# Kernel optimization log

Hardware: AMD Instinct MI355X
Metric: run time of the kernel (lower is better)

## Reference

```python
import jax, jax.numpy as jnp
import numpy as np

B, C, H, W = 64, 1, 512, 512
THRESHOLD = 50.0
LEVELS = 3


def _haar_dwt2(x):
    """Single-level 2D Haar DWT on [B,H,W] (even H,W). Returns (cA,(cH,cV,cD)).
    Matches pywt 'haar' coefficient magnitudes (sign conventions are irrelevant
    to the loss, which is odd-symmetric through soft-threshold and uses |.|)."""
    a = x[:, 0::2, 0::2]
    b = x[:, 0::2, 1::2]
    c = x[:, 1::2, 0::2]
    d = x[:, 1::2, 1::2]
    half = jnp.float32(0.5)
    cA = (a + b + c + d) * half
    cH = (a + b - c - d) * half  # low along cols, high along rows
    cV = (a - b + c - d) * half  # high along cols, low along rows
    cD = (a - b - c + d) * half  # high/high
    return cA, (cH, cV, cD)


def _wavedec2(x, levels):
    """Multi-level DWT. Returns detail tuples ordered coarsest-first,
    matching pywt.wavedec2 list order coeffs[1:]."""
    details = []
    cA = x
    for _ in range(levels):
        cA, d = _haar_dwt2(cA)
        details.append(d)
    details.reverse()  # coarsest first
    return details


def _soft_threshold(x, thr):
    return jnp.sign(x) * jnp.maximum(jnp.abs(x) - thr, 0.0)


def setup_inputs() -> dict:
    key = jax.random.key(0)
    k1, k2 = jax.random.split(key)
    pred = jax.random.uniform(k1, (B, C, H, W), dtype=jnp.float32)
    target = jax.random.uniform(k2, (B, C, H, W), dtype=jnp.float32)
    return {"pred": pred, "target": target}


def reference(pred, target):
    p = pred[:, 0]   # [B,H,W]
    t = target[:, 0]
    det_p = _wavedec2(p, LEVELS)
    det_t = _wavedec2(t, LEVELS)
    total = jnp.float32(0.0)
    for level_idx in range(1, LEVELS + 1):
        # per-level adaptive threshold, normalized to [0,1] image range
        thr = jnp.float32((THRESHOLD / 2.0 ** (level_idx - 1)) / 255.0)
        level_weight = jnp.float32(1.0 / level_idx)
        dp = det_p[level_idx - 1]
        dt = det_t[level_idx - 1]
        level_loss = jnp.float32(0.0)
        for k in range(3):  # cH, cV, cD
            diff = _soft_threshold(dp[k], thr) - _soft_threshold(dt[k], thr)
            level_loss = level_loss + jnp.mean(jnp.abs(diff))
        total = total + level_weight * level_loss / 3.0
    # per-sample sum / valid_samples == batch mean (all samples valid here)
    return total
```

## Files before the change

kernel.cpp:

```cpp
#include <hip/hip_runtime.h>


#define IMG_W 512
#define N_BATCH 64

#define THR1 (50.0f / 255.0f)
#define THR2 (25.0f / 255.0f)
#define THR3 (12.5f / 255.0f)

#define NBLK 1024
#define N_WAVES (NBLK * 4)
#define N_TILES 8192

__device__ __forceinline__ float softthr(float x, float thr) {
    float m = fmaxf(fabsf(x) - thr, 0.0f);
    return copysignf(m, x);
}

__device__ __forceinline__ float detail_term(float p, float t, float thr) {
    return fabsf(softthr(p, thr) - softthr(t, thr));
}

__device__ __forceinline__ void haar_quad(float a, float b, float c, float d,
                                          float& cA, float& cH, float& cV, float& cD) {
    cA = 0.5f * (a + b + c + d);
    cH = 0.5f * (a + b - c - d);
    cV = 0.5f * (a - b + c - d);
    cD = 0.5f * (a - b - c + d);
}

__device__ __forceinline__ float4 ld4(const float* p) { return *(const float4*)p; }

__global__ __launch_bounds__(256, 4)
void wavelet_main(const float* __restrict__ pred,
                  const float* __restrict__ target,
                  float* __restrict__ ws) {
    constexpr float W1 = 1.0f / (1.0f * 3.0f * (float)(N_BATCH * 256 * 256));
    constexpr float W2 = 1.0f / (2.0f * 3.0f * (float)(N_BATCH * 128 * 128));
    constexpr float W3 = 1.0f / (3.0f * 3.0f * (float)(N_BATCH * 64 * 64));

    const int wid = blockIdx.x * 4 + (threadIdx.x >> 6);
    const int li  = threadIdx.x & 63;

    float acc = 0.0f;

    #pragma unroll
    for (int t = 0; t < 2; ++t) {
        const int T     = wid + t * N_WAVES;
        const int img   = T >> 7;
        const int rem   = T & 127;
        const int half  = rem & 1;
        const int strip = rem >> 1;

        const size_t off = (size_t)img * (512 * 512)
                         + (size_t)strip * 8 * IMG_W
                         + half * 256 + 4 * li;
        const float* pb = pred + off;
        const float* tb = target + off;

        float4 Pa[2], Pb[2], Ta[2], Tb[2];
        Pa[0] = ld4(pb);            Pb[0] = ld4(pb + IMG_W);
        Ta[0] = ld4(tb);            Tb[0] = ld4(tb + IMG_W);
        Pa[1] = ld4(pb + 1024);     Pb[1] = ld4(pb + 1536);
        Ta[1] = ld4(tb + 1024);     Tb[1] = ld4(tb + 1536);

        float s1 = 0.0f, s2 = 0.0f;
        float cA1p[4][2], cA1t[4][2];

        #pragma unroll
        for (int rp = 0; rp < 4; ++rp) {
            const int bsel = rp & 1;
            const float4 p0 = Pa[bsel], p1 = Pb[bsel];
            const float4 q0 = Ta[bsel], q1 = Tb[bsel];

            if (rp < 2) {
                const int o = (rp + 2) * 1024;
                Pa[bsel] = ld4(pb + o);         Pb[bsel] = ld4(pb + o + IMG_W);
                Ta[bsel] = ld4(tb + o);         Tb[bsel] = ld4(tb + o + IMG_W);
            }

            float cA, cH, cV, cD, cAt, cHt, cVt, cDt;
            haar_quad(p0.x, p0.y, p1.x, p1.y, cA, cH, cV, cD);
            haar_quad(q0.x, q0.y, q1.x, q1.y, cAt, cHt, cVt, cDt);
            s1 += detail_term(cH, cHt, THR1) + detail_term(cV, cVt, THR1) + detail_term(cD, cDt, THR1);
            cA1p[rp][0] = cA; cA1t[rp][0] = cAt;
            haar_quad(p0.z, p0.w, p1.z, p1.w, cA, cH, cV, cD);
            haar_quad(q0.z, q0.w, q1.z, q1.w, cAt, cHt, cVt, cDt);
            s1 += detail_term(cH, cHt, THR1) + detail_term(cV, cVt, THR1) + detail_term(cD, cDt, THR1);
            cA1p[rp][1] = cA; cA1t[rp][1] = cAt;
        }

        float cA2p[2], cA2t[2];
        {
            float cH, cV, cD, cHt, cVt, cDt;
            haar_quad(cA1p[0][0], cA1p[0][1], cA1p[1][0], cA1p[1][1], cA2p[0], cH, cV, cD);
            haar_quad(cA1t[0][0], cA1t[0][1], cA1t[1][0], cA1t[1][1], cA2t[0], cHt, cVt, cDt);
            s2 += detail_term(cH, cHt, THR2) + detail_term(cV, cVt, THR2) + detail_term(cD, cDt, THR2);
            haar_quad(cA1p[2][0], cA1p[2][1], cA1p[3][0], cA1p[3][1], cA2p[1], cH, cV, cD);
            haar_quad(cA1t[2][0], cA1t[2][1], cA1t[3][0], cA1t[3][1], cA2t[1], cHt, cVt, cDt);
            s2 += detail_term(cH, cHt, THR2) + detail_term(cV, cVt, THR2) + detail_term(cD, cDt, THR2);
        }

        float s3;
        {
            const float bP = __shfl_xor(cA2p[0], 1);
            const float dP = __shfl_xor(cA2p[1], 1);
            const float bT = __shfl_xor(cA2t[0], 1);
            const float dT = __shfl_xor(cA2t[1], 1);
            float cA, cH, cV, cD, cAt, cHt, cVt, cDt;
            haar_quad(cA2p[0], bP, cA2p[1], dP, cA, cH, cV, cD);
            haar_quad(cA2t[0], bT, cA2t[1], dT, cAt, cHt, cVt, cDt);
            s3 = detail_term(cH, cHt, THR3) + detail_term(cV, cVt, THR3) + detail_term(cD, cDt, THR3);
        }
        const float w3 = (li & 1) ? 0.0f : W3;

        acc += W1 * s1 + W2 * s2 + w3 * s3;
    }

    #pragma unroll
    for (int off = 32; off > 0; off >>= 1)
        acc += __shfl_down(acc, off, 64);

    __shared__ float wave_sums[4];
    const int lane_b = threadIdx.x & 63;
    const int wave_b = threadIdx.x >> 6;
    if (lane_b == 0) wave_sums[wave_b] = acc;
    __syncthreads();
    if (threadIdx.x == 0)
        ws[blockIdx.x] = wave_sums[0] + wave_sums[1] + wave_sums[2] + wave_sums[3];
}

__global__ __launch_bounds__(256)
void wavelet_reduce(const float* __restrict__ ws, float* __restrict__ out) {
    const int tidx = threadIdx.x;
    float v = 0.0f;
    #pragma unroll
    for (int k = 0; k < NBLK / 256; ++k)
        v += ws[tidx + k * 256];

    #pragma unroll
    for (int off = 32; off > 0; off >>= 1)
        v += __shfl_down(v, off, 64);

    __shared__ float wave_sums[4];
    const int lane = tidx & 63;
    const int wave = tidx >> 6;
    if (lane == 0) wave_sums[wave] = v;
    __syncthreads();
    if (tidx == 0)
        out[0] = wave_sums[0] + wave_sums[1] + wave_sums[2] + wave_sums[3];
}

extern "C" void kernel_launch(void* const* d_in, const int* in_sizes, int n_in,
                              void* d_out, int out_size, void* d_ws, size_t ws_size,
                              hipStream_t stream) {
    const float* pred   = (const float*)d_in[0];
    const float* target = (const float*)d_in[1];
    float* out = (float*)d_out;
    float* ws  = (float*)d_ws;

    wavelet_main<<<NBLK, 256, 0, stream>>>(pred, target, ws);
    wavelet_reduce<<<1, 256, 0, stream>>>(ws, out);
}
```

Measured before the change: 143.9 us.

## Issue all tile loads upfront with nontemporal loads, one tile per wave

Each wave now handles a single 8-row strip tile instead of two. The grid is doubled to 2048 blocks and the launch-bounds occupancy hint is raised to 8. All 16 row loads per wave are issued at once through nontemporal vector loads, replacing the two-stage software-pipelined double buffer. The aim is more memory-level parallelism and streaming loads that bypass cache retention on a bandwidth-bound pass, at the cost of higher register pressure per thread and more blocks writing partial sums.

```diff
diff --git a/kernel.cpp b/kernel.cpp
--- a/kernel.cpp
+++ b/kernel.cpp
@@ -8,9 +8,9 @@
 #define THR2 (25.0f / 255.0f)
 #define THR3 (12.5f / 255.0f)
 
-#define NBLK 1024
-#define N_WAVES (NBLK * 4)
-#define N_TILES 8192
+#define NBLK 2048
+
+typedef float v4f __attribute__((ext_vector_type(4)));
 
 __device__ __forceinline__ float softthr(float x, float thr) {
     float m = fmaxf(fabsf(x) - thr, 0.0f);
@@ -29,9 +29,11 @@
     cD = 0.5f * (a - b - c + d);
 }
 
-__device__ __forceinline__ float4 ld4(const float* p) { return *(const float4*)p; }
+__device__ __forceinline__ v4f ld4nt(const float* p) {
+    return __builtin_nontemporal_load((const v4f*)p);
+}
 
-__global__ __launch_bounds__(256, 4)
+__global__ __launch_bounds__(256, 8)
 void wavelet_main(const float* __restrict__ pred,
                   const float* __restrict__ target,
                   float* __restrict__ ws) {
@@ -39,83 +41,81 @@
     constexpr float W2 = 1.0f / (2.0f * 3.0f * (float)(N_BATCH * 128 * 128));
     constexpr float W3 = 1.0f / (3.0f * 3.0f * (float)(N_BATCH * 64 * 64));
 
-    const int wid = blockIdx.x * 4 + (threadIdx.x >> 6);
-    const int li  = threadIdx.x & 63;
+    const int T  = blockIdx.x * 4 + (threadIdx.x >> 6);
+    const int li = threadIdx.x & 63;
 
-    float acc = 0.0f;
+    const int img   = T >> 7;
+    const int rem   = T & 127;
+    const int half  = rem & 1;
+    const int strip = rem >> 1;
 
-    #pragma unroll
-    for (int t = 0; t < 2; ++t) {
-        const int T     = wid + t * N_WAVES;
-        const int img   = T >> 7;
-        const int rem   = T & 127;
-        const int half  = rem & 1;
-        const int strip = rem >> 1;
+    const size_t off = (size_t)img * (512 * 512)
+                     + (size_t)strip * 8 * IMG_W
+                     + half * 256 + 4 * li;
+    const float* pb = pred + off;
+    const float* tb = target + off;
 
-        const size_t off = (size_t)img * (512 * 512)
-                         + (size_t)strip * 8 * IMG_W
-                         + half * 256 + 4 * li;
-        const float* pb = pred + off;
-        const float* tb = target + off;
+    v4f P0 = ld4nt(pb);                 v4f P1 = ld4nt(pb + IMG_W);
+    v4f P2 = ld4nt(pb + 2 * IMG_W);     v4f P3 = ld4nt(pb + 3 * IMG_W);
+    v4f P4 = ld4nt(pb + 4 * IMG_W);     v4f P5 = ld4nt(pb + 5 * IMG_W);
+    v4f P6 = ld4nt(pb + 6 * IMG_W);     v4f P7 = ld4nt(pb + 7 * IMG_W);
+    v4f Q0 = ld4nt(tb);                 v4f Q1 = ld4nt(tb + IMG_W);
+    v4f Q2 = ld4nt(tb + 2 * IMG_W);     v4f Q3 = ld4nt(tb + 3 * IMG_W);
+    v4f Q4 = ld4nt(tb + 4 * IMG_W);     v4f Q5 = ld4nt(tb + 5 * IMG_W);
+    v4f Q6 = ld4nt(tb + 6 * IMG_W);     v4f Q7 = ld4nt(tb + 7 * IMG_W);
 
-        float4 Pa[2], Pb[2], Ta[2], Tb[2];
-        Pa[0] = ld4(pb);            Pb[0] = ld4(pb + IMG_W);
-        Ta[0] = ld4(tb);            Tb[0] = ld4(tb + IMG_W);
-        Pa[1] = ld4(pb + 1024);     Pb[1] = ld4(pb + 1536);
-        Ta[1] = ld4(tb + 1024);     Tb[1] = ld4(tb + 1536);
+    float s1 = 0.0f, s2 = 0.0f;
+    float cA1p[4][2], cA1t[4][2];
 
-        float s1 = 0.0f, s2 = 0.0f;
-        float cA1p[4][2], cA1t[4][2];
+    {
+        float cA, cH, cV, cD, cAt, cHt, cVt, cDt;
 
-        #pragma unroll
-        for (int rp = 0; rp < 4; ++rp) {
-            const int bsel = rp & 1;
-            const float4 p0 = Pa[bsel], p1 = Pb[bsel];
-            const float4 q0 = Ta[bsel], q1 = Tb[bsel];
-
-            if (rp < 2) {
-                const int o = (rp + 2) * 1024;
-                Pa[bsel] = ld4(pb + o);         Pb[bsel] = ld4(pb + o + IMG_W);
-                Ta[bsel] = ld4(tb + o);         Tb[bsel] = ld4(tb + o + IMG_W);
-            }
-
-            float cA, cH, cV, cD, cAt, cHt, cVt, cDt;
-            haar_quad(p0.x, p0.y, p1.x, p1.y, cA, cH, cV, cD);
-            haar_quad(q0.x, q0.y, q1.x, q1.y, cAt, cHt, cVt, cDt);
-            s1 += detail_term(cH, cHt, THR1) + detail_term(cV, cVt, THR1) + detail_term(cD, cDt, THR1);
-            cA1p[rp][0] = cA; cA1t[rp][0] = cAt;
-            haar_quad(p0.z, p0.w, p1.z, p1.w, cA, cH, cV, cD);
-            haar_quad(q0.z, q0.w, q1.z, q1.w, cAt, cHt, cVt, cDt);
-            s1 += detail_term(cH, cHt, THR1) + detail_term(cV, cVt, THR1) + detail_term(cD, cDt, THR1);
-            cA1p[rp][1] = cA; cA1t[rp][1] = cAt;
+        #define L1_PAIR(a, b, qa, qb, rp)                                              \
+        {                                                                              \
+            haar_quad((a).x, (a).y, (b).x, (b).y, cA, cH, cV, cD);                     \
+            haar_quad((qa).x, (qa).y, (qb).x, (qb).y, cAt, cHt, cVt, cDt);             \
+            s1 += detail_term(cH, cHt, THR1) + detail_term(cV, cVt, THR1)              \
+                + detail_term(cD, cDt, THR1);                                          \
+            cA1p[rp][0] = cA; cA1t[rp][0] = cAt;                                       \
+            haar_quad((a).z, (a).w, (b).z, (b).w, cA, cH, cV, cD);                     \
+            haar_quad((qa).z, (qa).w, (qb).z, (qb).w, cAt, cHt, cVt, cDt);             \
+            s1 += detail_term(cH, cHt, THR1) + detail_term(cV, cVt, THR1)              \
+                + detail_term(cD, cDt, THR1);                                          \
+            cA1p[rp][1] = cA; cA1t[rp][1] = cAt;                                       \
         }
 
-        float cA2p[2], cA2t[2];
-        {
-            float cH, cV, cD, cHt, cVt, cDt;
-            haar_quad(cA1p[0][0], cA1p[0][1], cA1p[1][0], cA1p[1][1], cA2p[0], cH, cV, cD);
-            haar_quad(cA1t[0][0], cA1t[0][1], cA1t[1][0], cA1t[1][1], cA2t[0], cHt, cVt, cDt);
-            s2 += detail_term(cH, cHt, THR2) + detail_term(cV, cVt, THR2) + detail_term(cD, cDt, THR2);
-            haar_quad(cA1p[2][0], cA1p[2][1], cA1p[3][0], cA1p[3][1], cA2p[1], cH, cV, cD);
-            haar_quad(cA1t[2][0], cA1t[2][1], cA1t[3][0], cA1t[3][1], cA2t[1], cHt, cVt, cDt);
-            s2 += detail_term(cH, cHt, THR2) + detail_term(cV, cVt, THR2) + detail_term(cD, cDt, THR2);
-        }
+        L1_PAIR(P0, P1, Q0, Q1, 0)
+        L1_PAIR(P2, P3, Q2, Q3, 1)
+        L1_PAIR(P4, P5, Q4, Q5, 2)
+        L1_PAIR(P6, P7, Q6, Q7, 3)
+        #undef L1_PAIR
+    }
 
-        float s3;
-        {
-            const float bP = __shfl_xor(cA2p[0], 1);
-            const float dP = __shfl_xor(cA2p[1], 1);
-            const float bT = __shfl_xor(cA2t[0], 1);
-            const float dT = __shfl_xor(cA2t[1], 1);
-            float cA, cH, cV, cD, cAt, cHt, cVt, cDt;
-            haar_quad(cA2p[0], bP, cA2p[1], dP, cA, cH, cV, cD);
-            haar_quad(cA2t[0], bT, cA2t[1], dT, cAt, cHt, cVt, cDt);
-            s3 = detail_term(cH, cHt, THR3) + detail_term(cV, cVt, THR3) + detail_term(cD, cDt, THR3);
-        }
-        const float w3 = (li & 1) ? 0.0f : W3;
+    float cA2p[2], cA2t[2];
+    {
+        float cH, cV, cD, cHt, cVt, cDt;
+        haar_quad(cA1p[0][0], cA1p[0][1], cA1p[1][0], cA1p[1][1], cA2p[0], cH, cV, cD);
+        haar_quad(cA1t[0][0], cA1t[0][1], cA1t[1][0], cA1t[1][1], cA2t[0], cHt, cVt, cDt);
+        s2 += detail_term(cH, cHt, THR2) + detail_term(cV, cVt, THR2) + detail_term(cD, cDt, THR2);
+        haar_quad(cA1p[2][0], cA1p[2][1], cA1p[3][0], cA1p[3][1], cA2p[1], cH, cV, cD);
+        haar_quad(cA1t[2][0], cA1t[2][1], cA1t[3][0], cA1t[3][1], cA2t[1], cHt, cVt, cDt);
+        s2 += detail_term(cH, cHt, THR2) + detail_term(cV, cVt, THR2) + detail_term(cD, cDt, THR2);
+    }
 
-        acc += W1 * s1 + W2 * s2 + w3 * s3;
+    float s3;
+    {
+        const float bP = __shfl_xor(cA2p[0], 1);
+        const float dP = __shfl_xor(cA2p[1], 1);
+        const float bT = __shfl_xor(cA2t[0], 1);
+        const float dT = __shfl_xor(cA2t[1], 1);
+        float cA, cH, cV, cD, cAt, cHt, cVt, cDt;
+        haar_quad(cA2p[0], bP, cA2p[1], dP, cA, cH, cV, cD);
+        haar_quad(cA2t[0], bT, cA2t[1], dT, cAt, cHt, cVt, cDt);
+        s3 = detail_term(cH, cHt, THR3) + detail_term(cV, cVt, THR3) + detail_term(cD, cDt, THR3);
     }
+    const float w3 = (li & 1) ? 0.0f : W3;
+
+    float acc = W1 * s1 + W2 * s2 + w3 * s3;
 
     #pragma unroll
     for (int off = 32; off > 0; off >>= 1)
```

Result: faster. 137.9 us (-4.2%).
